# Kernel tuning notes

Measured on AMD Instinct MI355X. Metric: run time of the kernel, lower is better.

Reference implementation:

```python
import jax, jax.numpy as jnp
import numpy as np

VOCAB, EMB, HID = 32000, 1024, 1024
SEQ, BATCH = 512, 64


def setup_inputs() -> dict:
    key = jax.random.key(0)
    ks = jax.random.split(key, 8)
    inp = {
        "input": jax.random.randint(ks[0], (SEQ, BATCH), 0, VOCAB, dtype=jnp.int64)
        if jax.config.jax_enable_x64 else jax.random.randint(ks[0], (SEQ, BATCH), 0, VOCAB, dtype=jnp.int32),
        "input_lengths": jax.random.randint(ks[1], (BATCH,), 1, SEQ, dtype=jnp.int32),
        "hidden": jnp.zeros((1, BATCH, HID), dtype=jnp.float32),
        # parameters (xavier-ish scaled normals)
        "emb": jax.random.normal(ks[2], (VOCAB, EMB), dtype=jnp.float32) * (2.0 / (VOCAB + EMB)) ** 0.5,
        "W_ih": jax.random.normal(ks[3], (3 * HID, EMB), dtype=jnp.float32) * (1.0 / HID) ** 0.5,
        "W_hh": jax.random.normal(ks[4], (3 * HID, HID), dtype=jnp.float32) * (1.0 / HID) ** 0.5,
        "b_ih": jax.random.normal(ks[5], (3 * HID,), dtype=jnp.float32) * (1.0 / HID) ** 0.5,
        "b_hh": jax.random.normal(ks[6], (3 * HID,), dtype=jnp.float32) * (1.0 / HID) ** 0.5,
    }
    return inp


def _gru_scan(x, h0, W_ih, W_hh, b_ih, b_hh):
    # x: (T, B, D); h0: (B, H). PyTorch GRU gate math, gates ordered r, z, n.
    H = h0.shape[-1]

    def step(h, x_t):
        gi = x_t @ W_ih.T + b_ih          # (B, 3H)
        gh = h @ W_hh.T + b_hh            # (B, 3H)
        i_r, i_z, i_n = gi[:, :H], gi[:, H:2 * H], gi[:, 2 * H:]
        h_r, h_z, h_n = gh[:, :H], gh[:, H:2 * H], gh[:, 2 * H:]
        r = jax.nn.sigmoid(i_r + h_r)
        z = jax.nn.sigmoid(i_z + h_z)
        n = jnp.tanh(i_n + r * h_n)
        h_new = (1.0 - z) * n + z * h
        return h_new, h_new

    _, hs = jax.lax.scan(step, h0, x)
    return hs  # (T, B, H)


def reference(input, input_lengths, hidden, emb, W_ih, W_hh, b_ih, b_hh):
    # embedded: (T, B, D); input_lengths is unused by the original forward.
    embedded = emb[input]
    h0 = hidden[0]  # num_layers == 1
    hiddens = _gru_scan(embedded, h0, W_ih, W_hh, b_ih, b_hh)
    # torch.stack(hidden_list, 0).squeeze(1) with num_layers=1 -> (T, B, H)
    return hiddens
```

## Files before the change

### kernel.cpp

```cpp
#include <hip/hip_runtime.h>

typedef short bhalf8 __attribute__((ext_vector_type(8)));
typedef float f32x4  __attribute__((ext_vector_type(4)));

__device__ __forceinline__ unsigned short f2bf(float f) {
    unsigned int u = __builtin_bit_cast(unsigned int, f);
    u = (u + 0x7fffu + ((u >> 16) & 1u)) >> 16;
    return (unsigned short)u;
}
__device__ __forceinline__ float bf2f(unsigned short h) {
    unsigned int u = ((unsigned int)h) << 16;
    return __builtin_bit_cast(float, u);
}

__device__ __forceinline__ bhalf8 ldg16_bypass(const unsigned short* p) {
    bhalf8 r;
    asm volatile("global_load_dwordx4 %0, %1, off sc0 sc1"
                 : "=v"(r) : "v"(p));
    return r;
}

#define VWAIT(N)                                                     \
    do {                                                             \
        asm volatile("s_waitcnt vmcnt(" #N ")" ::: "memory");        \
        __builtin_amdgcn_sched_barrier(0);                           \
    } while (0)

#define SEQ   512
#define BATCH 64
#define HID   1024
#define EMBD  1024
#define VOCAB 32000
#define N3H   3072
#define NBLK  64
#define FLAGSTRIDE 32

__global__ void k_cvt4(const float4* __restrict__ in, ushort4* __restrict__ out, int n4) {
    int i = blockIdx.x * blockDim.x + threadIdx.x;
    if (i < n4) {
        float4 v = in[i];
        ushort4 o;
        o.x = f2bf(v.x); o.y = f2bf(v.y); o.z = f2bf(v.z); o.w = f2bf(v.w);
        out[i] = o;
    }
}

__global__ __launch_bounds__(256)
void k_gi(const int* __restrict__ tok, const unsigned short* __restrict__ embb,
          const unsigned short* __restrict__ wih, unsigned short* __restrict__ gi) {
    int nb = blockIdx.x;
    int mb = blockIdx.y;
    int w    = threadIdx.x >> 6;
    int lane = threadIdx.x & 63;
    int q = lane >> 4, l = lane & 15;
    int m0 = mb * 256 + w * 16;
    int n0 = nb * 64;

    const unsigned short* ap[4];
#pragma unroll
    for (int i = 0; i < 4; ++i)
        ap[i] = embb + (size_t)tok[m0 + 64 * i + l] * EMBD + q * 8;

    const unsigned short* bp[4];
#pragma unroll
    for (int j = 0; j < 4; ++j)
        bp[j] = wih + (size_t)(n0 + 16 * j + l) * EMBD + q * 8;

    f32x4 acc[4][4];
#pragma unroll
    for (int i = 0; i < 4; ++i)
#pragma unroll
        for (int j = 0; j < 4; ++j)
            acc[i][j] = (f32x4){0.f, 0.f, 0.f, 0.f};

#pragma unroll 2
    for (int kk = 0; kk < 32; ++kk) {
        int ko = kk * 32;
        bhalf8 bv[4], av[4];
#pragma unroll
        for (int j = 0; j < 4; ++j) bv[j] = *(const bhalf8*)(bp[j] + ko);
#pragma unroll
        for (int i = 0; i < 4; ++i) av[i] = *(const bhalf8*)(ap[i] + ko);
#pragma unroll
        for (int i = 0; i < 4; ++i)
#pragma unroll
            for (int j = 0; j < 4; ++j)
                acc[i][j] = __builtin_amdgcn_mfma_f32_16x16x32_bf16(av[i], bv[j], acc[i][j], 0, 0, 0);
    }
#pragma unroll
    for (int i = 0; i < 4; ++i)
#pragma unroll
        for (int r = 0; r < 4; ++r) {
            size_t mrow = (size_t)(m0 + 64 * i + q * 4 + r) * N3H + n0;
            gi[mrow +  0 + l] = f2bf(acc[i][0][r]);
            gi[mrow + 16 + l] = f2bf(acc[i][1][r]);
            gi[mrow + 32 + l] = f2bf(acc[i][2][r]);
            gi[mrow + 48 + l] = f2bf(acc[i][3][r]);
        }
}

__device__ __forceinline__ void gbar(int* flags, int e) {
    __syncthreads();
    if (threadIdx.x == 0)
        __hip_atomic_store(flags + (size_t)blockIdx.x * FLAGSTRIDE, e,
                           __ATOMIC_RELAXED, __HIP_MEMORY_SCOPE_AGENT);
    if (threadIdx.x < 64) {
        for (;;) {
            int v = __hip_atomic_load(flags + (size_t)threadIdx.x * FLAGSTRIDE,
                                      __ATOMIC_RELAXED, __HIP_MEMORY_SCOPE_AGENT);
            if (__all(v >= e)) break;
            __builtin_amdgcn_s_sleep(1);
        }
    }
    __syncthreads();
}

__global__ __launch_bounds__(256, 1)
void k_rec(const float* __restrict__ W_hh,
           const unsigned short* __restrict__ gib,
           const float* __restrict__ bih, const float* __restrict__ bhh,
           const float* __restrict__ hidden,
           float* __restrict__ out,
           unsigned short* hbuf,
           int* flags) {
    __shared__ unsigned short sh[32768];

    const int tid  = threadIdx.x;
    const int w    = tid >> 6;
    const int lane = tid & 63;
    const int q = lane >> 4, l = lane & 15;
    const int G  = blockIdx.x;
    const int m0 = w * 16;
    const int u0 = G * 16 + l;

    for (int i = 0; i < 16; ++i) {
        int c  = i * 256 + tid;
        int g  = c >> 11;
        int kk = (c >> 6) & 31;
        int ln = c & 63;
        int uu = ln & 15, qq = ln >> 4;
        const float* src = W_hh + (size_t)(g * 1024 + G * 16 + uu) * 1024 + kk * 32 + qq * 8;
        float4 f0 = *(const float4*)src;
        float4 f1 = *(const float4*)(src + 4);
        ushort4 o0, o1;
        o0.x = f2bf(f0.x); o0.y = f2bf(f0.y); o0.z = f2bf(f0.z); o0.w = f2bf(f0.w);
        o1.x = f2bf(f1.x); o1.y = f2bf(f1.y); o1.z = f2bf(f1.z); o1.w = f2bf(f1.w);
        *(ushort4*)&sh[c * 8]     = o0;
        *(ushort4*)&sh[c * 8 + 4] = o1;
    }

    bhalf8 bn[32];
#pragma unroll
    for (int kk = 0; kk < 32; ++kk) {
        const float* src = W_hh + (size_t)(2048 + u0) * 1024 + kk * 32 + q * 8;
        float4 f0 = *(const float4*)src;
        float4 f1 = *(const float4*)(src + 4);
        bhalf8 v;
        v[0] = (short)f2bf(f0.x); v[1] = (short)f2bf(f0.y);
        v[2] = (short)f2bf(f0.z); v[3] = (short)f2bf(f0.w);
        v[4] = (short)f2bf(f1.x); v[5] = (short)f2bf(f1.y);
        v[6] = (short)f2bf(f1.z); v[7] = (short)f2bf(f1.w);
        bn[kk] = v;
    }

    float hp[4];
#pragma unroll
    for (int r = 0; r < 4; ++r) {
        int b = m0 + q * 4 + r;
        float hv = hidden[(size_t)b * HID + u0];
        hp[r] = hv;
        __hip_atomic_store(hbuf + (size_t)b * HID + u0, f2bf(hv),
                           __ATOMIC_RELAXED, __HIP_MEMORY_SCOPE_AGENT);
    }
    float bir = bih[u0], biz = bih[HID + u0], bin = bih[2 * HID + u0];
    float bhr = bhh[u0], bhz = bhh[HID + u0], bhn = bhh[2 * HID + u0];

    float i_r[4], i_z[4], i_n[4];
#pragma unroll
    for (int r = 0; r < 4; ++r) {
        const unsigned short* gp = gib + (size_t)(m0 + q * 4 + r) * N3H + u0;
        i_r[r] = bf2f(gp[0])       + bir;
        i_z[r] = bf2f(gp[HID])     + biz;
        i_n[r] = bf2f(gp[2 * HID]) + bin;
    }

    gbar(flags, 1);

#define ISSUE8(AV, KB)                                                   \
    _Pragma("unroll")                                                    \
    for (int j = 0; j < 8; ++j) AV[j] = ldg16_bypass(hA + ((KB) + j) * 32);

#define COMPUTE8(AV, KB)                                                 \
    _Pragma("unroll")                                                    \
    for (int j = 0; j < 8; ++j) {                                        \
        int kk = (KB) + j;                                               \
        bhalf8 brf = *(const bhalf8*)&sh[kk * 512 + lane * 8];           \
        bhalf8 bzf = *(const bhalf8*)&sh[16384 + kk * 512 + lane * 8];   \
        ar = __builtin_amdgcn_mfma_f32_16x16x32_bf16(AV[j], brf, ar, 0, 0, 0); \
        az = __builtin_amdgcn_mfma_f32_16x16x32_bf16(AV[j], bzf, az, 0, 0, 0); \
        an = __builtin_amdgcn_mfma_f32_16x16x32_bf16(AV[j], bn[kk], an, 0, 0, 0); \
    }

    for (int t = 0; t < SEQ; ++t) {
        const unsigned short* hc = hbuf + (size_t)(t & 1) * (BATCH * HID);
        unsigned short*       hn = hbuf + (size_t)((t + 1) & 1) * (BATCH * HID);

        unsigned short pr[4], pz[4], pn[4];
        if (t + 1 < SEQ) {
            const unsigned short* gt = gib + (size_t)(t + 1) * (BATCH * N3H);
#pragma unroll
            for (int r = 0; r < 4; ++r) {
                const unsigned short* gp = gt + (size_t)(m0 + q * 4 + r) * N3H + u0;
                pr[r] = gp[0]; pz[r] = gp[HID]; pn[r] = gp[2 * HID];
            }
        }

        const unsigned short* hA = hc + (size_t)(m0 + l) * HID + q * 8;
        f32x4 ar = {0.f, 0.f, 0.f, 0.f}, az = ar, an = ar;

        {
            bhalf8 ha[8], hb[8];
            ISSUE8(ha, 0)
            ISSUE8(hb, 8)
            VWAIT(8);
            COMPUTE8(ha, 0)
            ISSUE8(ha, 16)
            VWAIT(8);
            COMPUTE8(hb, 8)
            ISSUE8(hb, 24)
            VWAIT(8);
            COMPUTE8(ha, 16)
            VWAIT(0);
            COMPUTE8(hb, 24)
        }

        float osv[4];
#pragma unroll
        for (int r = 0; r < 4; ++r) {
            int b = m0 + q * 4 + r;
            float rr = 1.f / (1.f + __expf(-(i_r[r] + ar[r] + bhr)));
            float zz = 1.f / (1.f + __expf(-(i_z[r] + az[r] + bhz)));
            float nn = tanhf(i_n[r] + rr * (an[r] + bhn));
            float hv = (1.f - zz) * nn + zz * hp[r];
            hp[r] = hv;
            osv[r] = hv;
            if (t + 1 < SEQ)
                __hip_atomic_store(hn + (size_t)b * HID + u0, f2bf(hv),
                                   __ATOMIC_RELAXED, __HIP_MEMORY_SCOPE_AGENT);
        }

        if (t + 1 < SEQ) {
#pragma unroll
            for (int r = 0; r < 4; ++r) {
                i_r[r] = bf2f(pr[r]) + bir;
                i_z[r] = bf2f(pz[r]) + biz;
                i_n[r] = bf2f(pn[r]) + bin;
            }
            gbar(flags, t + 2);
        }

        float* ot = out + (size_t)t * (BATCH * HID);
#pragma unroll
        for (int r = 0; r < 4; ++r)
            __builtin_nontemporal_store(osv[r], &ot[(size_t)(m0 + q * 4 + r) * HID + u0]);
    }
#undef ISSUE8
#undef COMPUTE8
}

extern "C" void kernel_launch(void* const* d_in, const int* in_sizes, int n_in,
                              void* d_out, int out_size, void* d_ws, size_t ws_size,
                              hipStream_t stream) {
    (void)in_sizes; (void)n_in; (void)out_size;
    const int*   input  = (const int*)  d_in[0];
    const float* hidden = (const float*)d_in[2];
    const float* emb    = (const float*)d_in[3];
    const float* W_ih   = (const float*)d_in[4];
    const float* W_hh   = (const float*)d_in[5];
    const float* b_ih   = (const float*)d_in[6];
    const float* b_hh   = (const float*)d_in[7];
    float* out = (float*)d_out;

    const size_t EMB_BF  = 0;
    const size_t WIH_BF  = EMB_BF + (size_t)VOCAB * EMBD * 2;
    const size_t GI_OFF  = WIH_BF + (size_t)N3H * EMBD * 2;
    const size_t H_OFF   = GI_OFF + (size_t)SEQ * BATCH * N3H * 2;
    const size_t FLG_OFF = H_OFF + (size_t)2 * BATCH * HID * 2;
    const size_t NEED    = FLG_OFF + (size_t)NBLK * FLAGSTRIDE * 4;
    if (ws_size < NEED) return;

    char* ws = (char*)d_ws;
    unsigned short* embb = (unsigned short*)(ws + EMB_BF);
    unsigned short* wihb = (unsigned short*)(ws + WIH_BF);
    unsigned short* gib  = (unsigned short*)(ws + GI_OFF);
    unsigned short* hbuf = (unsigned short*)(ws + H_OFF);
    int*            flags = (int*)(ws + FLG_OFF);

    hipMemsetAsync(flags, 0, (size_t)NBLK * FLAGSTRIDE * 4, stream);

    {
        int n4 = VOCAB * EMBD / 4;
        k_cvt4<<<(n4 + 255) / 256, 256, 0, stream>>>((const float4*)emb, (ushort4*)embb, n4);
    }
    {
        int n4 = N3H * EMBD / 4;
        k_cvt4<<<(n4 + 255) / 256, 256, 0, stream>>>((const float4*)W_ih, (ushort4*)wihb, n4);
    }

    k_gi<<<dim3(48, 128), 256, 0, stream>>>(input, embb, wihb, gib);

    k_rec<<<NBLK, 256, 0, stream>>>(W_hh, gib, b_ih, b_hh, hidden, out, hbuf, flags);
}
```

Before: 4.279 ms.

## Streamline GRU recurrence barrier, loads, and stores; remap GEMM blocks per XCD

Every wave now polls the step flags itself instead of one wave polling followed by a second block sync. Hidden-state stores use a write-through short store instead of an atomic. Next-step gate-input loads are issued as inline asm after the first hidden-state loads, and the wait counts are adjusted to match. tanh is replaced with an exp-based formula. The output store is no longer nontemporal, and the k_gi grid is flattened with an XCD-aware mapping of block index to tile. These changes aim to cut per-step synchronisation and latency, but the hand-written waitcnt values and the weaker memory ordering add correctness risk.

After: 4.014 ms. -6.2%, faster.

```diff
diff --git a/kernel.cpp b/kernel.cpp
--- a/kernel.cpp
+++ b/kernel.cpp
@@ -15,9 +15,12 @@
 
 __device__ __forceinline__ bhalf8 ldg16_bypass(const unsigned short* p) {
     bhalf8 r;
-    asm volatile("global_load_dwordx4 %0, %1, off sc0 sc1"
-                 : "=v"(r) : "v"(p));
+    asm volatile("global_load_dwordx4 %0, %1, off sc0 sc1" : "=v"(r) : "v"(p));
     return r;
+}
+__device__ __forceinline__ void stg2_wt(unsigned short* p, unsigned short v) {
+    unsigned int vv = v;
+    asm volatile("global_store_short %0, %1, off sc0 sc1" :: "v"(p), "v"(vv) : "memory");
 }
 
 #define VWAIT(N)                                                     \
@@ -48,8 +51,11 @@
 __global__ __launch_bounds__(256)
 void k_gi(const int* __restrict__ tok, const unsigned short* __restrict__ embb,
           const unsigned short* __restrict__ wih, unsigned short* __restrict__ gi) {
-    int nb = blockIdx.x;
-    int mb = blockIdx.y;
+    int g   = blockIdx.x;
+    int xcd = g & 7;
+    int j   = g >> 3;
+    int mb  = xcd * 16 + (j / 48);
+    int nb  = j % 48;
     int w    = threadIdx.x >> 6;
     int lane = threadIdx.x & 63;
     int q = lane >> 4, l = lane & 15;
@@ -63,29 +69,29 @@
 
     const unsigned short* bp[4];
 #pragma unroll
-    for (int j = 0; j < 4; ++j)
-        bp[j] = wih + (size_t)(n0 + 16 * j + l) * EMBD + q * 8;
+    for (int jj = 0; jj < 4; ++jj)
+        bp[jj] = wih + (size_t)(n0 + 16 * jj + l) * EMBD + q * 8;
 
     f32x4 acc[4][4];
 #pragma unroll
     for (int i = 0; i < 4; ++i)
 #pragma unroll
-        for (int j = 0; j < 4; ++j)
-            acc[i][j] = (f32x4){0.f, 0.f, 0.f, 0.f};
+        for (int jj = 0; jj < 4; ++jj)
+            acc[i][jj] = (f32x4){0.f, 0.f, 0.f, 0.f};
 
 #pragma unroll 2
     for (int kk = 0; kk < 32; ++kk) {
         int ko = kk * 32;
         bhalf8 bv[4], av[4];
 #pragma unroll
-        for (int j = 0; j < 4; ++j) bv[j] = *(const bhalf8*)(bp[j] + ko);
+        for (int jj = 0; jj < 4; ++jj) bv[jj] = *(const bhalf8*)(bp[jj] + ko);
 #pragma unroll
         for (int i = 0; i < 4; ++i) av[i] = *(const bhalf8*)(ap[i] + ko);
 #pragma unroll
         for (int i = 0; i < 4; ++i)
 #pragma unroll
-            for (int j = 0; j < 4; ++j)
-                acc[i][j] = __builtin_amdgcn_mfma_f32_16x16x32_bf16(av[i], bv[j], acc[i][j], 0, 0, 0);
+            for (int jj = 0; jj < 4; ++jj)
+                acc[i][jj] = __builtin_amdgcn_mfma_f32_16x16x32_bf16(av[i], bv[jj], acc[i][jj], 0, 0, 0);
     }
 #pragma unroll
     for (int i = 0; i < 4; ++i)
@@ -104,15 +110,13 @@
     if (threadIdx.x == 0)
         __hip_atomic_store(flags + (size_t)blockIdx.x * FLAGSTRIDE, e,
                            __ATOMIC_RELAXED, __HIP_MEMORY_SCOPE_AGENT);
-    if (threadIdx.x < 64) {
-        for (;;) {
-            int v = __hip_atomic_load(flags + (size_t)threadIdx.x * FLAGSTRIDE,
-                                      __ATOMIC_RELAXED, __HIP_MEMORY_SCOPE_AGENT);
-            if (__all(v >= e)) break;
-            __builtin_amdgcn_s_sleep(1);
-        }
-    }
-    __syncthreads();
+    int lane = threadIdx.x & 63;
+    for (;;) {
+        int v = __hip_atomic_load(flags + (size_t)lane * FLAGSTRIDE,
+                                  __ATOMIC_RELAXED, __HIP_MEMORY_SCOPE_AGENT);
+        if (__all(v >= e)) break;
+        __builtin_amdgcn_s_sleep(1);
+    }
 }
 
 __global__ __launch_bounds__(256, 1)
@@ -135,11 +139,11 @@
 
     for (int i = 0; i < 16; ++i) {
         int c  = i * 256 + tid;
-        int g  = c >> 11;
+        int gg = c >> 11;
         int kk = (c >> 6) & 31;
         int ln = c & 63;
         int uu = ln & 15, qq = ln >> 4;
-        const float* src = W_hh + (size_t)(g * 1024 + G * 16 + uu) * 1024 + kk * 32 + qq * 8;
+        const float* src = W_hh + (size_t)(gg * 1024 + G * 16 + uu) * 1024 + kk * 32 + qq * 8;
         float4 f0 = *(const float4*)src;
         float4 f1 = *(const float4*)(src + 4);
         ushort4 o0, o1;
@@ -167,10 +171,9 @@
 #pragma unroll
     for (int r = 0; r < 4; ++r) {
         int b = m0 + q * 4 + r;
-        float hv = hidden[(size_t)b * HID + u0];
-        hp[r] = hv;
-        __hip_atomic_store(hbuf + (size_t)b * HID + u0, f2bf(hv),
-                           __ATOMIC_RELAXED, __HIP_MEMORY_SCOPE_AGENT);
+        float hv0 = hidden[(size_t)b * HID + u0];
+        hp[r] = hv0;
+        stg2_wt(hbuf + (size_t)b * HID + u0, f2bf(hv0));
     }
     float bir = bih[u0], biz = bih[HID + u0], bin = bih[2 * HID + u0];
     float bhr = bhh[u0], bhz = bhh[HID + u0], bhn = bhh[2 * HID + u0];
@@ -188,51 +191,49 @@
 
 #define ISSUE8(AV, KB)                                                   \
     _Pragma("unroll")                                                    \
-    for (int j = 0; j < 8; ++j) AV[j] = ldg16_bypass(hA + ((KB) + j) * 32);
+    for (int jj = 0; jj < 8; ++jj) AV[jj] = ldg16_bypass(hA + ((KB) + jj) * 32);
 
 #define COMPUTE8(AV, KB)                                                 \
     _Pragma("unroll")                                                    \
-    for (int j = 0; j < 8; ++j) {                                        \
-        int kk = (KB) + j;                                               \
+    for (int jj = 0; jj < 8; ++jj) {                                     \
+        int kk = (KB) + jj;                                              \
         bhalf8 brf = *(const bhalf8*)&sh[kk * 512 + lane * 8];           \
         bhalf8 bzf = *(const bhalf8*)&sh[16384 + kk * 512 + lane * 8];   \
-        ar = __builtin_amdgcn_mfma_f32_16x16x32_bf16(AV[j], brf, ar, 0, 0, 0); \
-        az = __builtin_amdgcn_mfma_f32_16x16x32_bf16(AV[j], bzf, az, 0, 0, 0); \
-        an = __builtin_amdgcn_mfma_f32_16x16x32_bf16(AV[j], bn[kk], an, 0, 0, 0); \
+        ar = __builtin_amdgcn_mfma_f32_16x16x32_bf16(AV[jj], brf, ar, 0, 0, 0); \
+        az = __builtin_amdgcn_mfma_f32_16x16x32_bf16(AV[jj], bzf, az, 0, 0, 0); \
+        an = __builtin_amdgcn_mfma_f32_16x16x32_bf16(AV[jj], bn[kk], an, 0, 0, 0); \
     }
 
     for (int t = 0; t < SEQ; ++t) {
         const unsigned short* hc = hbuf + (size_t)(t & 1) * (BATCH * HID);
         unsigned short*       hn = hbuf + (size_t)((t + 1) & 1) * (BATCH * HID);
-
-        unsigned short pr[4], pz[4], pn[4];
-        if (t + 1 < SEQ) {
-            const unsigned short* gt = gib + (size_t)(t + 1) * (BATCH * N3H);
+        const unsigned short* hA = hc + (size_t)(m0 + l) * HID + q * 8;
+
+        f32x4 ar = {0.f, 0.f, 0.f, 0.f}, az = ar, an = ar;
+
+        bhalf8 ha[8], hb[8];
+        ISSUE8(ha, 0)
+        ISSUE8(hb, 8)
+
+        unsigned int pr[4], pz[4], pn[4];
+        {
+            const unsigned short* gt = gib +
+                (size_t)((t + 1 < SEQ) ? (t + 1) : t) * (BATCH * N3H);
 #pragma unroll
             for (int r = 0; r < 4; ++r) {
-                const unsigned short* gp = gt + (size_t)(m0 + q * 4 + r) * N3H + u0;
-                pr[r] = gp[0]; pz[r] = gp[HID]; pn[r] = gp[2 * HID];
+                const unsigned short* gp = gt + (size_t)(m0 + q * 4 + r) * N3H + u0 + HID;
+                asm volatile("global_load_ushort %0, %1, off offset:-2048" : "=v"(pr[r]) : "v"(gp));
+                asm volatile("global_load_ushort %0, %1, off"              : "=v"(pz[r]) : "v"(gp));
+                asm volatile("global_load_ushort %0, %1, off offset:2048"  : "=v"(pn[r]) : "v"(gp));
             }
         }
 
-        const unsigned short* hA = hc + (size_t)(m0 + l) * HID + q * 8;
-        f32x4 ar = {0.f, 0.f, 0.f, 0.f}, az = ar, an = ar;
-
-        {
-            bhalf8 ha[8], hb[8];
-            ISSUE8(ha, 0)
-            ISSUE8(hb, 8)
-            VWAIT(8);
-            COMPUTE8(ha, 0)
-            ISSUE8(ha, 16)
-            VWAIT(8);
-            COMPUTE8(hb, 8)
-            ISSUE8(hb, 24)
-            VWAIT(8);
-            COMPUTE8(ha, 16)
-            VWAIT(0);
-            COMPUTE8(hb, 24)
-        }
+        VWAIT(20);  COMPUTE8(ha, 0)
+        ISSUE8(ha, 16)
+        VWAIT(20);  COMPUTE8(hb, 8)
+        ISSUE8(hb, 24)
+        VWAIT(8);   COMPUTE8(ha, 16)
+        VWAIT(0);   COMPUTE8(hb, 24)
 
         float osv[4];
 #pragma unroll
@@ -240,29 +241,29 @@
             int b = m0 + q * 4 + r;
             float rr = 1.f / (1.f + __expf(-(i_r[r] + ar[r] + bhr)));
             float zz = 1.f / (1.f + __expf(-(i_z[r] + az[r] + bhz)));
-            float nn = tanhf(i_n[r] + rr * (an[r] + bhn));
-            float hv = (1.f - zz) * nn + zz * hp[r];
-            hp[r] = hv;
-            osv[r] = hv;
+            float targ = i_n[r] + rr * (an[r] + bhn);
+            float ex   = __expf(-2.f * targ);
+            float nn   = (1.f - ex) / (1.f + ex);
+            float hv2 = (1.f - zz) * nn + zz * hp[r];
+            hp[r] = hv2;
+            osv[r] = hv2;
             if (t + 1 < SEQ)
-                __hip_atomic_store(hn + (size_t)b * HID + u0, f2bf(hv),
-                                   __ATOMIC_RELAXED, __HIP_MEMORY_SCOPE_AGENT);
+                stg2_wt(hn + (size_t)b * HID + u0, f2bf(hv2));
         }
 
-        if (t + 1 < SEQ) {
-#pragma unroll
-            for (int r = 0; r < 4; ++r) {
-                i_r[r] = bf2f(pr[r]) + bir;
-                i_z[r] = bf2f(pz[r]) + biz;
-                i_n[r] = bf2f(pn[r]) + bin;
-            }
-            gbar(flags, t + 2);
+#pragma unroll
+        for (int r = 0; r < 4; ++r) {
+            i_r[r] = bf2f((unsigned short)pr[r]) + bir;
+            i_z[r] = bf2f((unsigned short)pz[r]) + biz;
+            i_n[r] = bf2f((unsigned short)pn[r]) + bin;
         }
 
+        if (t + 1 < SEQ) gbar(flags, t + 2);
+
         float* ot = out + (size_t)t * (BATCH * HID);
 #pragma unroll
         for (int r = 0; r < 4; ++r)
-            __builtin_nontemporal_store(osv[r], &ot[(size_t)(m0 + q * 4 + r) * HID + u0]);
+            ot[(size_t)(m0 + q * 4 + r) * HID + u0] = osv[r];
     }
 #undef ISSUE8
 #undef COMPUTE8
@@ -284,17 +285,17 @@
     const size_t EMB_BF  = 0;
     const size_t WIH_BF  = EMB_BF + (size_t)VOCAB * EMBD * 2;
     const size_t GI_OFF  = WIH_BF + (size_t)N3H * EMBD * 2;
-    const size_t H_OFF   = GI_OFF + (size_t)SEQ * BATCH * N3H * 2;
-    const size_t FLG_OFF = H_OFF + (size_t)2 * BATCH * HID * 2;
-    const size_t NEED    = FLG_OFF + (size_t)NBLK * FLAGSTRIDE * 4;
+    const size_t FLG_OFF = GI_OFF + (size_t)SEQ * BATCH * N3H * 2;
+    const size_t H_OFF   = FLG_OFF + (size_t)NBLK * FLAGSTRIDE * 4;
+    const size_t NEED    = H_OFF + (size_t)2 * BATCH * HID * 2;
     if (ws_size < NEED) return;
 
     char* ws = (char*)d_ws;
     unsigned short* embb = (unsigned short*)(ws + EMB_BF);
     unsigned short* wihb = (unsigned short*)(ws + WIH_BF);
     unsigned short* gib  = (unsigned short*)(ws + GI_OFF);
+    int*            flags = (int*)(ws + FLG_OFF);
     unsigned short* hbuf = (unsigned short*)(ws + H_OFF);
-    int*            flags = (int*)(ws + FLG_OFF);
 
     hipMemsetAsync(flags, 0, (size_t)NBLK * FLAGSTRIDE * 4, stream);
 
@@ -307,7 +308,7 @@
         k_cvt4<<<(n4 + 255) / 256, 256, 0, stream>>>((const float4*)W_ih, (ushort4*)wihb, n4);
     }
 
-    k_gi<<<dim3(48, 128), 256, 0, stream>>>(input, embb, wihb, gib);
+    k_gi<<<6144, 256, 0, stream>>>(input, embb, wihb, gib);
 
     k_rec<<<NBLK, 256, 0, stream>>>(W_hh, gib, b_ih, b_hh, hidden, out, hbuf, flags);
 }
```
